# Performance work log

Hardware: AMD Instinct MI355X
Metric: run time of the kernel (lower is better)

Reference implementation:

```python
import jax, jax.numpy as jnp
import numpy as np

EMBED_DIM = 1024
NUM_HEADS = 16
HEAD_DIM = EMBED_DIM // NUM_HEADS
BITS = 8


def quantize_bits(x, bits):
    # Faithful min-max fake quantization from the original module.
    qmax = 2 ** bits - 1
    x_min = x.min()
    x_max = x.max()
    scale = (x_max - x_min) / (qmax + 1e-08)
    x_q = jnp.round(jnp.clip((x - x_min) / (scale + 1e-08), 0, qmax))
    return x_q * scale + x_min


def rope_sin_cos(seq_len, dim):
    # inv_freq over half the head dim, matching RotaryEmbedding's freqs table.
    inv_freq = 1.0 / 10000 ** (jnp.arange(0, dim, 2, dtype=jnp.float32) / dim)
    t = jnp.arange(seq_len, dtype=jnp.float32)
    freqs = t[:, None] * inv_freq[None, :]  # (S, D/2)
    return jnp.sin(freqs), jnp.cos(freqs)


def apply_rotary(x, sin, cos):
    # x: (B, H, S, D); sin/cos: (1, 1, S, D/2)
    x1, x2 = jnp.split(x, 2, axis=-1)
    return jnp.concatenate([x1 * cos - x2 * sin, x1 * sin + x2 * cos], axis=-1)


def setup_inputs() -> dict:
    key = jax.random.key(0)
    k1, k2, k3 = jax.random.split(key, 3)
    B, S, E = 2, 2048, EMBED_DIM
    x = jax.random.normal(k1, (B, S, E), dtype=jnp.float32)
    # lecun_normal-style init: std = 1/sqrt(fan_in)
    w_qkv = jax.random.normal(k2, (E, 3 * E), dtype=jnp.float32) / np.sqrt(E)
    w_out = jax.random.normal(k3, (E, E), dtype=jnp.float32) / np.sqrt(E)
    return {"x": x, "w_qkv": w_qkv, "w_out": w_out}


def reference(x, w_qkv, w_out):
    B, S, E = x.shape
    H, D = NUM_HEADS, HEAD_DIM
    # Fake-quantized QKV projection
    qkv = x @ quantize_bits(w_qkv, BITS)                    # (B, S, 3E)
    qkv = qkv.reshape(B, S, 3, H, D)
    q = qkv[:, :, 0].transpose(0, 2, 1, 3)                  # (B, H, S, D)
    k = qkv[:, :, 1].transpose(0, 2, 1, 3)
    v = qkv[:, :, 2].transpose(0, 2, 1, 3)
    sin, cos = rope_sin_cos(S, D)
    sin = sin[None, None]
    cos = cos[None, None]
    q = apply_rotary(q, sin, cos)
    k = apply_rotary(k, sin, cos)
    scores = jnp.einsum('bhqd,bhkd->bhqk', q, k) / jnp.sqrt(jnp.float32(D))
    attn = jax.nn.softmax(scores, axis=-1)                  # (B, H, S, S)
    out = jnp.einsum('bhqk,bhkd->bhqd', attn, v)            # (B, H, S, D)
    out = out.transpose(0, 2, 1, 3).reshape(B, S, E)
    return out @ quantize_bits(w_out, BITS)
```

## Files before the change

kernel.cpp:

```cpp
#include <hip/hip_runtime.h>
#include <hip/hip_bf16.h>

typedef __bf16 bf16;
typedef bf16  bf16x8 __attribute__((ext_vector_type(8)));
typedef bf16  bf16x4 __attribute__((ext_vector_type(4)));
typedef bf16  bf16x2 __attribute__((ext_vector_type(2)));
typedef float f32x4  __attribute__((ext_vector_type(4)));
typedef float f32x16 __attribute__((ext_vector_type(16)));
typedef int   i32x4  __attribute__((ext_vector_type(4)));

#define MFMA16(a,b,c) __builtin_amdgcn_mfma_f32_16x16x32_bf16((a),(b),(c),0,0,0)
#define MFMA32(a,b,c) __builtin_amdgcn_mfma_f32_32x32x16_bf16((a),(b),(c),0,0,0)

#define GLDS16(gp, lp) __builtin_amdgcn_global_load_lds( \
    (const __attribute__((address_space(1))) void*)(void*)(gp), \
    (__attribute__((address_space(3))) void*)(lp), 16, 0, 0)

static __device__ __forceinline__ bf16x8 lds_frag(const char* p){
  i32x4 v = *(const i32x4*)p;
  return __builtin_bit_cast(bf16x8, v);
}
static __device__ __forceinline__ bf16x8 g_frag(const bf16* p){
  i32x4 v = *(const i32x4*)p;
  return __builtin_bit_cast(bf16x8, v);
}
static __device__ __forceinline__ unsigned pk_bf16(float a, float b){
  bf16x2 v = { (bf16)a, (bf16)b };
  return __builtin_bit_cast(unsigned, v);
}
static __device__ __forceinline__ void p32swap(unsigned &a, unsigned &b){
  asm("v_permlane32_swap_b32 %0, %1" : "+v"(a), "+v"(b));
}

__device__ __forceinline__ unsigned fmap(float f){
  unsigned u = __float_as_uint(f);
  return (u & 0x80000000u) ? ~u : (u | 0x80000000u);
}
__device__ __forceinline__ float funmap(unsigned m){
  unsigned u = (m & 0x80000000u) ? (m & 0x7FFFFFFFu) : ~m;
  return __uint_as_float(u);
}

__global__ void init_mm(unsigned* mm){
  if (threadIdx.x == 0){
    mm[0] = 0xFFFFFFFFu; mm[1] = 0u;
    mm[2] = 0xFFFFFFFFu; mm[3] = 0u;
  }
}

__global__ void minmax_k(const float* __restrict__ w, int n, unsigned* __restrict__ mm){
  __shared__ unsigned smn[256], smx[256];
  int tid = threadIdx.x;
  unsigned lmn = 0xFFFFFFFFu, lmx = 0u;
  for (int i = blockIdx.x * blockDim.x + tid; i < n; i += gridDim.x * blockDim.x){
    unsigned u = fmap(w[i]);
    lmn = min(lmn, u); lmx = max(lmx, u);
  }
  smn[tid] = lmn; smx[tid] = lmx;
  __syncthreads();
  for (int s = 128; s > 0; s >>= 1){
    if (tid < s){
      smn[tid] = min(smn[tid], smn[tid + s]);
      smx[tid] = max(smx[tid], smx[tid + s]);
    }
    __syncthreads();
  }
  if (tid == 0){ atomicMin(&mm[0], smn[0]); atomicMax(&mm[1], smx[0]); }
}

__global__ void dq_t(const float* __restrict__ w, bf16* __restrict__ wt,
                     int R, int C, const unsigned* __restrict__ mm){
  __shared__ float t[32][33];
  float xmin = funmap(mm[0]);
  float xmax = funmap(mm[1]);
  float scale = (xmax - xmin) / 255.0f;
  float denom = scale + 1e-8f;
  int ct = blockIdx.x * 32, rt = blockIdx.y * 32;
  int tx = threadIdx.x, ty = threadIdx.y;
#pragma unroll
  for (int p = 0; p < 4; ++p){
    int r = rt + p * 8 + ty;
    float x = w[(size_t)r * C + ct + tx];
    float q = rintf(fminf(fmaxf((x - xmin) / denom, 0.0f), 255.0f));
    t[p * 8 + ty][tx] = q * scale + xmin;
  }
  __syncthreads();
#pragma unroll
  for (int p = 0; p < 4; ++p){
    int c = p * 8 + ty;
    wt[(size_t)(ct + c) * R + rt + tx] = (bf16)t[tx][c];
  }
}

__global__ void cast_x(const float* __restrict__ x, bf16* __restrict__ xb, int n4){
  int i = blockIdx.x * 256 + threadIdx.x;
  if (i < n4){
    f32x4 v = *(const f32x4*)(x + (size_t)i * 4);
    bf16x4 o = { (bf16)v.x, (bf16)v.y, (bf16)v.z, (bf16)v.w };
    *(bf16x4*)(xb + (size_t)i * 4) = o;
  }
}

__global__ void sincos_k(float* __restrict__ sintab, float* __restrict__ costab){
  int idx = blockIdx.x * 256 + threadIdx.x;
  int i = idx & 31, s = idx >> 5;
  float invf = powf(10000.0f, -(float)i / 32.0f);
  float fr = (float)s * invf;
  sintab[idx] = sinf(fr);
  costab[idx] = cosf(fr);
}

__global__ void rope_qk(const float* __restrict__ qkv,
                        const float* __restrict__ sintab, const float* __restrict__ costab,
                        bf16* __restrict__ Qr, bf16* __restrict__ Kr){
  int idx = blockIdx.x * 256 + threadIdx.x;
  int i  = idx & 31;
  int s  = (idx >> 5) & 2047;
  int bh = idx >> 16;
  int b = bh >> 4, h = bh & 15;
  const float QS = 0.18033688011f;
  const float* row = qkv + (size_t)(b * 2048 + s) * 3072 + h * 64;
  float q1 = row[i],        q2 = row[32 + i];
  float k1 = row[1024 + i], k2 = row[1024 + 32 + i];
  float sn = sintab[s * 32 + i], cs = costab[s * 32 + i];
  size_t o = ((size_t)bh * 2048 + s) * 64 + i;
  Qr[o]      = (bf16)((q1 * cs - q2 * sn) * QS);
  Qr[o + 32] = (bf16)((q1 * sn + q2 * cs) * QS);
  Kr[o]      = (bf16)(k1 * cs - k2 * sn);
  Kr[o + 32] = (bf16)(k1 * sn + k2 * cs);
}

__global__ void vtrans(const float* __restrict__ qkv, bf16* __restrict__ Vt){
  __shared__ float t[64][65];
  int bh = blockIdx.x >> 5;
  int st = (blockIdx.x & 31) * 64;
  int b = bh >> 4, h = bh & 15;
  int tx = threadIdx.x & 63, ty4 = threadIdx.x >> 6;
#pragma unroll
  for (int p = 0; p < 16; ++p){
    int s = p * 4 + ty4;
    t[s][tx] = qkv[(size_t)(b * 2048 + st + s) * 3072 + 2048 + h * 64 + tx];
  }
  __syncthreads();
#pragma unroll
  for (int p = 0; p < 16; ++p){
    int d = p * 4 + ty4;
    Vt[((size_t)bh * 64 + d) * 2048 + st + tx] = (bf16)t[tx][d];
  }
}

__global__ __launch_bounds__(256, 2) void gemm_bt(
    const bf16* __restrict__ A, const bf16* __restrict__ Bt,
    float* __restrict__ C, int M, int N, int K)
{
  __shared__ __align__(16) char lds[32768];
  int nbx = N >> 7;
  int bid = blockIdx.x;
  int nwg = gridDim.x;
  if ((nwg & 7) == 0){ int q = nwg >> 3; bid = (bid & 7) * q + (bid >> 3); }
  int row0 = (bid / nbx) << 7;
  int col0 = (bid % nbx) << 7;
  int tid = threadIdx.x, lane = tid & 63, wid = tid >> 6;
  int wr = (wid >> 1) * 64, wc = (wid & 1) * 64;
  int lr = lane & 15, g = lane >> 4;

  int aoff[2][4], boff[2][4];
#pragma unroll
  for (int kk = 0; kk < 2; ++kk){
#pragma unroll
    for (int m = 0; m < 4; ++m){
      int ra = wr + m * 16 + lr;
      aoff[kk][m] = ra * 128 + ((((kk * 4 + g) ^ ((ra >> 1) & 7))) << 4);
      int rb = wc + m * 16 + lr;
      boff[kk][m] = 16384 + rb * 128 + ((((kk * 4 + g) ^ ((rb >> 1) & 7))) << 4);
    }
  }

  const bf16* pA[4]; const bf16* pB[4]; int loff[4];
#pragma unroll
  for (int is = 0; is < 4; ++is){
    int f = is * 4096 + wid * 1024 + lane * 16;
    int r = f >> 7, c = (f >> 4) & 7;
    int cg = c ^ ((r >> 1) & 7);
    pA[is] = A  + (size_t)(row0 + r) * K + cg * 8;
    pB[is] = Bt + (size_t)(col0 + r) * K + cg * 8;
    loff[is] = is * 4096 + wid * 1024;
  }

  f32x4 acc[4][4] = {};
  for (int kt = 0; kt < K; kt += 64){
    __syncthreads();
#pragma unroll
    for (int is = 0; is < 4; ++is){
      GLDS16(pA[is] + kt, lds + loff[is]);
      GLDS16(pB[is] + kt, lds + 16384 + loff[is]);
    }
    __syncthreads();
#pragma unroll
    for (int kk = 0; kk < 2; ++kk){
      bf16x8 af[4], bfb[4];
#pragma unroll
      for (int m = 0; m < 4; ++m) af[m] = lds_frag(lds + aoff[kk][m]);
#pragma unroll
      for (int n = 0; n < 4; ++n) bfb[n] = lds_frag(lds + boff[kk][n]);
#pragma unroll
      for (int m = 0; m < 4; ++m)
#pragma unroll
        for (int n = 0; n < 4; ++n)
          acc[m][n] = MFMA16(af[m], bfb[n], acc[m][n]);
    }
  }

#pragma unroll
  for (int m = 0; m < 4; ++m){
    int row = row0 + wr + m * 16 + g * 4;
#pragma unroll
    for (int n = 0; n < 4; ++n){
      int col = col0 + wc + n * 16 + lr;
      float* cp = C + (size_t)row * N + col;
#pragma unroll
      for (int r = 0; r < 4; ++r)
        cp[(size_t)r * N] = acc[m][n][r];
    }
  }
}

__global__ __launch_bounds__(256, 2) void attn_k(
    const bf16* __restrict__ Q, const bf16* __restrict__ K,
    const bf16* __restrict__ Vt, bf16* __restrict__ AO)
{
  __shared__ __align__(16) char kl[8192];
  __shared__ __align__(16) char vl[8192];

  int bid = blockIdx.x;
  bid = (bid & 7) * 64 + (bid >> 3);
  int bh = bid >> 4, qblk = bid & 15;
  int b = bh >> 4, h = bh & 15;
  int tid = threadIdx.x, lane = tid & 63, wid = tid >> 6;
  int l31 = lane & 31, hi = lane >> 5, hi8 = hi * 8;
  int q0 = qblk * 128 + wid * 32;

  const bf16* Qb = Q  + ((size_t)bh * 2048 + q0) * 64;
  const bf16* Kb = K  + (size_t)bh * 2048 * 64;
  const bf16* Vb = Vt + (size_t)bh * 64 * 2048;

  bf16x8 qf[4];
#pragma unroll
  for (int t = 0; t < 4; ++t)
    qf[t] = g_frag(Qb + (size_t)l31 * 64 + t * 16 + hi8);

  const bf16* pKs[2]; const bf16* pVs[2]; int ldo[2];
#pragma unroll
  for (int is = 0; is < 2; ++is){
    int f = wid * 2048 + is * 1024 + lane * 16;
    int r = f >> 7;
    int cg = ((f >> 4) & 7) ^ (r & 7);
    pKs[is] = Kb + (size_t)r * 64 + cg * 8;
    pVs[is] = Vb + (size_t)r * 2048 + cg * 8;
    ldo[is] = wid * 2048 + is * 1024;
  }

  f32x16 o0 = {}, o1 = {};
  float mrun = -1e30f, lrun = 0.0f;

  for (int c = 0; c < 32; ++c){
    int kv0 = c * 64;
    __syncthreads();
#pragma unroll
    for (int is = 0; is < 2; ++is){
      GLDS16(pKs[is] + (size_t)kv0 * 64, kl + ldo[is]);
      GLDS16(pVs[is] + kv0,              vl + ldo[is]);
    }
    __syncthreads();

#pragma unroll
    for (int kk = 0; kk < 2; ++kk){
      int krow = kk * 32 + l31;
      bf16x8 kf[4], vfr[4];
#pragma unroll
      for (int t = 0; t < 4; ++t)
        kf[t] = lds_frag(kl + krow * 128 + ((((2 * t + hi) ^ (krow & 7))) << 4));
#pragma unroll
      for (int u = 0; u < 4; ++u){
        int d = (u & 1) * 32 + l31;
        vfr[u] = lds_frag(vl + d * 128 +
                          ((((kk * 4) + ((u >> 1) * 2) + hi) ^ (d & 7)) << 4));
      }
      f32x16 sc = {};
#pragma unroll
      for (int t = 0; t < 4; ++t) sc = MFMA32(kf[t], qf[t], sc);

      float a0 = fmaxf(sc[0], sc[1]),   a1 = fmaxf(sc[2], sc[3]);
      float a2 = fmaxf(sc[4], sc[5]),   a3 = fmaxf(sc[6], sc[7]);
      float a4 = fmaxf(sc[8], sc[9]),   a5 = fmaxf(sc[10], sc[11]);
      float a6 = fmaxf(sc[12], sc[13]), a7 = fmaxf(sc[14], sc[15]);
      a0 = fmaxf(a0, a1); a2 = fmaxf(a2, a3);
      a4 = fmaxf(a4, a5); a6 = fmaxf(a6, a7);
      float mt = fmaxf(fmaxf(a0, a2), fmaxf(a4, a6));
      if (!__all(mt - mrun <= 8.0f)){
        mt = fmaxf(mt, __shfl_xor(mt, 32));
        float mn = fmaxf(mrun, mt);
        float cr = __builtin_amdgcn_exp2f(mrun - mn);
#pragma unroll
        for (int r = 0; r < 16; ++r){ o0[r] *= cr; o1[r] *= cr; }
        lrun *= cr; mrun = mn;
      }
#pragma unroll
      for (int r = 0; r < 16; ++r) sc[r] = __builtin_amdgcn_exp2f(sc[r] - mrun);
      float s0 = (sc[0] + sc[1]) + (sc[2] + sc[3]);
      float s1 = (sc[4] + sc[5]) + (sc[6] + sc[7]);
      float s2 = (sc[8] + sc[9]) + (sc[10] + sc[11]);
      float s3 = (sc[12] + sc[13]) + (sc[14] + sc[15]);
      lrun += (s0 + s1) + (s2 + s3);

#pragma unroll
      for (int kh = 0; kh < 2; ++kh){
        unsigned pa0 = pk_bf16(sc[kh * 8 + 0], sc[kh * 8 + 1]);
        unsigned pa1 = pk_bf16(sc[kh * 8 + 2], sc[kh * 8 + 3]);
        unsigned pb0 = pk_bf16(sc[kh * 8 + 4], sc[kh * 8 + 5]);
        unsigned pb1 = pk_bf16(sc[kh * 8 + 6], sc[kh * 8 + 7]);
        p32swap(pa0, pb0); p32swap(pa1, pb1);
        i32x4 wv = { (int)pa0, (int)pa1, (int)pb0, (int)pb1 };
        bf16x8 pf = __builtin_bit_cast(bf16x8, wv);
        o0 = MFMA32(vfr[kh * 2 + 0], pf, o0);
        o1 = MFMA32(vfr[kh * 2 + 1], pf, o1);
      }
    }
  }

  float lt = lrun + __shfl_xor(lrun, 32);
  float inv = 1.0f / lt;
  size_t row = (size_t)b * 2048 + q0 + l31;
  bf16* op = AO + row * 1024 + h * 64 + hi * 4;
#pragma unroll
  for (int qd = 0; qd < 4; ++qd){
    bf16x4 w0 = { (bf16)(o0[qd*4+0]*inv), (bf16)(o0[qd*4+1]*inv),
                  (bf16)(o0[qd*4+2]*inv), (bf16)(o0[qd*4+3]*inv) };
    *(bf16x4*)(op + qd * 8) = w0;
    bf16x4 w1 = { (bf16)(o1[qd*4+0]*inv), (bf16)(o1[qd*4+1]*inv),
                  (bf16)(o1[qd*4+2]*inv), (bf16)(o1[qd*4+3]*inv) };
    *(bf16x4*)(op + 32 + qd * 8) = w1;
  }
}

extern "C" void kernel_launch(void* const* d_in, const int* in_sizes, int n_in,
                              void* d_out, int out_size, void* d_ws, size_t ws_size,
                              hipStream_t stream) {
  const float* x     = (const float*)d_in[0];
  const float* w_qkv = (const float*)d_in[1];
  const float* w_out = (const float*)d_in[2];
  float* out = (float*)d_out;

  char* ws = (char*)d_ws;
  const size_t MB = 1u << 20;
  unsigned* mm   = (unsigned*)(ws);
  float* sintab  = (float*)(ws + 256);
  float* costab  = (float*)(ws + 256 + 262144);
  bf16* xb       = (bf16*)(ws + 1 * MB);
  bf16* wqkvT    = (bf16*)(ws + 9 * MB);
  bf16* woutT    = (bf16*)(ws + 15 * MB);
  float* qkvf    = (float*)(ws + 17 * MB);
  bf16* Qr       = (bf16*)(ws + 65 * MB);
  bf16* Kr       = (bf16*)(ws + 73 * MB);
  bf16* Vt       = (bf16*)(ws + 81 * MB);
  bf16* AO       = (bf16*)(ws + 1 * MB);

  init_mm<<<1, 64, 0, stream>>>(mm);
  minmax_k<<<512, 256, 0, stream>>>(w_qkv, 1024 * 3072, mm);
  minmax_k<<<512, 256, 0, stream>>>(w_out, 1024 * 1024, mm + 2);
  sincos_k<<<256, 256, 0, stream>>>(sintab, costab);
  cast_x<<<4096, 256, 0, stream>>>(x, xb, 4194304 / 4);
  dq_t<<<dim3(96, 32), dim3(32, 8), 0, stream>>>(w_qkv, wqkvT, 1024, 3072, mm);
  dq_t<<<dim3(32, 32), dim3(32, 8), 0, stream>>>(w_out, woutT, 1024, 1024, mm + 2);
  gemm_bt<<<768, 256, 0, stream>>>(xb, wqkvT, qkvf, 4096, 3072, 1024);
  rope_qk<<<8192, 256, 0, stream>>>(qkvf, sintab, costab, Qr, Kr);
  vtrans<<<1024, 256, 0, stream>>>(qkvf, Vt);
  attn_k<<<512, 256, 0, stream>>>(Qr, Kr, Vt, AO);
  gemm_bt<<<256, 256, 0, stream>>>(AO, woutT, out, 4096, 1024, 1024);

  (void)in_sizes; (void)n_in; (void)out_size; (void)ws_size;
}
```

Measured before the change: 171.9 us.

## Fuse RoPE into QKV GEMM epilogue and split attention KV across waves

```diff
diff --git a/kernel.cpp b/kernel.cpp
--- a/kernel.cpp
+++ b/kernel.cpp
@@ -101,45 +101,24 @@
   }
 }
 
-__global__ void sincos_k(float* __restrict__ sintab, float* __restrict__ costab){
+__global__ void sincos_k(float2* __restrict__ sctab){
   int idx = blockIdx.x * 256 + threadIdx.x;
   int i = idx & 31, s = idx >> 5;
   float invf = powf(10000.0f, -(float)i / 32.0f);
   float fr = (float)s * invf;
-  sintab[idx] = sinf(fr);
-  costab[idx] = cosf(fr);
-}
-
-__global__ void rope_qk(const float* __restrict__ qkv,
-                        const float* __restrict__ sintab, const float* __restrict__ costab,
-                        bf16* __restrict__ Qr, bf16* __restrict__ Kr){
-  int idx = blockIdx.x * 256 + threadIdx.x;
-  int i  = idx & 31;
-  int s  = (idx >> 5) & 2047;
-  int bh = idx >> 16;
-  int b = bh >> 4, h = bh & 15;
-  const float QS = 0.18033688011f;
-  const float* row = qkv + (size_t)(b * 2048 + s) * 3072 + h * 64;
-  float q1 = row[i],        q2 = row[32 + i];
-  float k1 = row[1024 + i], k2 = row[1024 + 32 + i];
-  float sn = sintab[s * 32 + i], cs = costab[s * 32 + i];
-  size_t o = ((size_t)bh * 2048 + s) * 64 + i;
-  Qr[o]      = (bf16)((q1 * cs - q2 * sn) * QS);
-  Qr[o + 32] = (bf16)((q1 * sn + q2 * cs) * QS);
-  Kr[o]      = (bf16)(k1 * cs - k2 * sn);
-  Kr[o + 32] = (bf16)(k1 * sn + k2 * cs);
-}
-
-__global__ void vtrans(const float* __restrict__ qkv, bf16* __restrict__ Vt){
+  float2 cs; cs.x = cosf(fr); cs.y = sinf(fr);
+  sctab[idx] = cs;
+}
+
+__global__ void vtrans_b(const bf16* __restrict__ Vraw, bf16* __restrict__ Vt){
   __shared__ float t[64][65];
   int bh = blockIdx.x >> 5;
   int st = (blockIdx.x & 31) * 64;
-  int b = bh >> 4, h = bh & 15;
   int tx = threadIdx.x & 63, ty4 = threadIdx.x >> 6;
 #pragma unroll
   for (int p = 0; p < 16; ++p){
     int s = p * 4 + ty4;
-    t[s][tx] = qkv[(size_t)(b * 2048 + st + s) * 3072 + 2048 + h * 64 + tx];
+    t[s][tx] = (float)Vraw[((size_t)bh * 2048 + st + s) * 64 + tx];
   }
   __syncthreads();
 #pragma unroll
@@ -225,51 +204,161 @@
   }
 }
 
-__global__ __launch_bounds__(256, 2) void attn_k(
+__global__ __launch_bounds__(256, 2) void gemm_qkv(
+    const bf16* __restrict__ A, const bf16* __restrict__ Bt,
+    const float2* __restrict__ sctab,
+    bf16* __restrict__ Qr, bf16* __restrict__ Kr, bf16* __restrict__ Vraw,
+    int M, int N, int K)
+{
+  __shared__ __align__(16) char lds[32768];
+  int nbx = N >> 7;
+  int bid = blockIdx.x;
+  int nwg = gridDim.x;
+  if ((nwg & 7) == 0){ int q = nwg >> 3; bid = (bid & 7) * q + (bid >> 3); }
+  int row0 = (bid / nbx) << 7;
+  int col0 = (bid % nbx) << 7;
+  int tid = threadIdx.x, lane = tid & 63, wid = tid >> 6;
+  int wr = (wid >> 1) * 64, wc = (wid & 1) * 64;
+  int lr = lane & 15, g = lane >> 4;
+
+  int aoff[2][4], boff[2][4];
+#pragma unroll
+  for (int kk = 0; kk < 2; ++kk){
+#pragma unroll
+    for (int m = 0; m < 4; ++m){
+      int ra = wr + m * 16 + lr;
+      aoff[kk][m] = ra * 128 + ((((kk * 4 + g) ^ ((ra >> 1) & 7))) << 4);
+      int rb = wc + m * 16 + lr;
+      boff[kk][m] = 16384 + rb * 128 + ((((kk * 4 + g) ^ ((rb >> 1) & 7))) << 4);
+    }
+  }
+
+  const bf16* pA[4]; const bf16* pB[4]; int loff[4];
+#pragma unroll
+  for (int is = 0; is < 4; ++is){
+    int f = is * 4096 + wid * 1024 + lane * 16;
+    int r = f >> 7, c = (f >> 4) & 7;
+    int cg = c ^ ((r >> 1) & 7);
+    pA[is] = A  + (size_t)(row0 + r) * K + cg * 8;
+    pB[is] = Bt + (size_t)(col0 + r) * K + cg * 8;
+    loff[is] = is * 4096 + wid * 1024;
+  }
+
+  f32x4 acc[4][4] = {};
+  for (int kt = 0; kt < K; kt += 64){
+    __syncthreads();
+#pragma unroll
+    for (int is = 0; is < 4; ++is){
+      GLDS16(pA[is] + kt, lds + loff[is]);
+      GLDS16(pB[is] + kt, lds + 16384 + loff[is]);
+    }
+    __syncthreads();
+#pragma unroll
+    for (int kk = 0; kk < 2; ++kk){
+      bf16x8 af[4], bfb[4];
+#pragma unroll
+      for (int m = 0; m < 4; ++m) af[m] = lds_frag(lds + aoff[kk][m]);
+#pragma unroll
+      for (int n = 0; n < 4; ++n) bfb[n] = lds_frag(lds + boff[kk][n]);
+#pragma unroll
+      for (int m = 0; m < 4; ++m)
+#pragma unroll
+        for (int n = 0; n < 4; ++n)
+          acc[m][n] = MFMA16(af[m], bfb[n], acc[m][n]);
+    }
+  }
+
+  int head = (col0 + wc) >> 6;
+  int sect = head >> 4;
+  int h = head & 15;
+  const float QS = 0.18033688011f;
+
+  if (sect == 2){
+#pragma unroll
+    for (int m = 0; m < 4; ++m){
+#pragma unroll
+      for (int r = 0; r < 4; ++r){
+        int s = row0 + wr + m * 16 + g * 4 + r;
+        int b = s >> 11, s2 = s & 2047;
+        bf16* vp = Vraw + (((size_t)(b * 16 + h)) * 2048 + s2) * 64;
+#pragma unroll
+        for (int n = 0; n < 4; ++n)
+          vp[n * 16 + lr] = (bf16)acc[m][n][r];
+      }
+    }
+  } else {
+    bf16* dst = sect ? Kr : Qr;
+    float scl = sect ? 1.0f : QS;
+#pragma unroll
+    for (int m = 0; m < 4; ++m){
+#pragma unroll
+      for (int r = 0; r < 4; ++r){
+        int s = row0 + wr + m * 16 + g * 4 + r;
+        int b = s >> 11, s2 = s & 2047;
+        bf16* qp = dst + (((size_t)(b * 16 + h)) * 2048 + s2) * 64;
+#pragma unroll
+        for (int n = 0; n < 2; ++n){
+          float x1 = acc[m][n][r], x2 = acc[m][n + 2][r];
+          float2 cs = sctab[s2 * 32 + n * 16 + lr];
+          qp[n * 16 + lr]      = (bf16)((x1 * cs.x - x2 * cs.y) * scl);
+          qp[n * 16 + lr + 32] = (bf16)((x1 * cs.y + x2 * cs.x) * scl);
+        }
+      }
+    }
+  }
+}
+
+__global__ __launch_bounds__(256, 4) void attn_k(
     const bf16* __restrict__ Q, const bf16* __restrict__ K,
     const bf16* __restrict__ Vt, bf16* __restrict__ AO)
 {
-  __shared__ __align__(16) char kl[8192];
-  __shared__ __align__(16) char vl[8192];
+  __shared__ __align__(16) char SB[32768];
+  __shared__ float mlds[4][2][32];
+  __shared__ float invL[2][32];
 
   int bid = blockIdx.x;
-  bid = (bid & 7) * 64 + (bid >> 3);
-  int bh = bid >> 4, qblk = bid & 15;
+  bid = (bid & 7) * 128 + (bid >> 3);
+  int bh = bid >> 5, qb = bid & 31;
   int b = bh >> 4, h = bh & 15;
   int tid = threadIdx.x, lane = tid & 63, wid = tid >> 6;
   int l31 = lane & 31, hi = lane >> 5, hi8 = hi * 8;
-  int q0 = qblk * 128 + wid * 32;
+  int qt = wid >> 1, half = wid & 1;
+  int q0 = qb * 64 + qt * 32;
 
   const bf16* Qb = Q  + ((size_t)bh * 2048 + q0) * 64;
   const bf16* Kb = K  + (size_t)bh * 2048 * 64;
   const bf16* Vb = Vt + (size_t)bh * 64 * 2048;
+  const bf16* Kh = Kb + (size_t)half * 1024 * 64;
+  int vcol0 = half * 1024;
 
   bf16x8 qf[4];
 #pragma unroll
   for (int t = 0; t < 4; ++t)
     qf[t] = g_frag(Qb + (size_t)l31 * 64 + t * 16 + hi8);
 
-  const bf16* pKs[2]; const bf16* pVs[2]; int ldo[2];
-#pragma unroll
-  for (int is = 0; is < 2; ++is){
-    int f = wid * 2048 + is * 1024 + lane * 16;
+  const bf16* pKs[4]; const bf16* pVs[4]; int ldo[4];
+#pragma unroll
+  for (int is = 0; is < 4; ++is){
+    int f = qt * 4096 + is * 1024 + lane * 16;
     int r = f >> 7;
     int cg = ((f >> 4) & 7) ^ (r & 7);
-    pKs[is] = Kb + (size_t)r * 64 + cg * 8;
-    pVs[is] = Vb + (size_t)r * 2048 + cg * 8;
-    ldo[is] = wid * 2048 + is * 1024;
-  }
+    pKs[is] = Kh + (size_t)r * 64 + cg * 8;
+    pVs[is] = Vb + (size_t)r * 2048 + vcol0 + cg * 8;
+    ldo[is] = qt * 4096 + is * 1024;
+  }
+  char* klh = SB + half * 8192;
+  char* vlh = SB + 16384 + half * 8192;
 
   f32x16 o0 = {}, o1 = {};
   float mrun = -1e30f, lrun = 0.0f;
 
-  for (int c = 0; c < 32; ++c){
+  for (int c = 0; c < 16; ++c){
     int kv0 = c * 64;
     __syncthreads();
 #pragma unroll
-    for (int is = 0; is < 2; ++is){
-      GLDS16(pKs[is] + (size_t)kv0 * 64, kl + ldo[is]);
-      GLDS16(pVs[is] + kv0,              vl + ldo[is]);
+    for (int is = 0; is < 4; ++is){
+      GLDS16(pKs[is] + (size_t)kv0 * 64, klh + ldo[is]);
+      GLDS16(pVs[is] + kv0,              vlh + ldo[is]);
     }
     __syncthreads();
 
@@ -279,11 +368,11 @@
       bf16x8 kf[4], vfr[4];
 #pragma unroll
       for (int t = 0; t < 4; ++t)
-        kf[t] = lds_frag(kl + krow * 128 + ((((2 * t + hi) ^ (krow & 7))) << 4));
+        kf[t] = lds_frag(klh + krow * 128 + ((((2 * t + hi) ^ (krow & 7))) << 4));
 #pragma unroll
       for (int u = 0; u < 4; ++u){
         int d = (u & 1) * 32 + l31;
-        vfr[u] = lds_frag(vl + d * 128 +
+        vfr[u] = lds_frag(vlh + d * 128 +
                           ((((kk * 4) + ((u >> 1) * 2) + hi) ^ (d & 7)) << 4));
       }
       f32x16 sc = {};
@@ -328,19 +417,45 @@
     }
   }
 
-  float lt = lrun + __shfl_xor(lrun, 32);
-  float inv = 1.0f / lt;
-  size_t row = (size_t)b * 2048 + q0 + l31;
-  bf16* op = AO + row * 1024 + h * 64 + hi * 4;
-#pragma unroll
-  for (int qd = 0; qd < 4; ++qd){
-    bf16x4 w0 = { (bf16)(o0[qd*4+0]*inv), (bf16)(o0[qd*4+1]*inv),
-                  (bf16)(o0[qd*4+2]*inv), (bf16)(o0[qd*4+3]*inv) };
-    *(bf16x4*)(op + qd * 8) = w0;
-    bf16x4 w1 = { (bf16)(o1[qd*4+0]*inv), (bf16)(o1[qd*4+1]*inv),
-                  (bf16)(o1[qd*4+2]*inv), (bf16)(o1[qd*4+3]*inv) };
-    *(bf16x4*)(op + 32 + qd * 8) = w1;
-  }
+  lrun += __shfl_xor(lrun, 32);
+
+  __syncthreads();
+  if (lane < 32){ mlds[wid][0][l31] = mrun; mlds[wid][1][l31] = lrun; }
+  __syncthreads();
+  float mp = mlds[wid ^ 1][0][l31];
+  float M = fmaxf(mrun, mp);
+  float ew = __builtin_amdgcn_exp2f(mrun - M);
+  if (half == 0 && lane < 32){
+    float lp = mlds[wid ^ 1][1][l31];
+    invL[qt][l31] = 1.0f / (lrun * ew + lp * __builtin_amdgcn_exp2f(mp - M));
+  }
+  float* Ow = (float*)SB + wid * 2048;
+#pragma unroll
+  for (int r = 0; r < 16; ++r){
+    int d = 8 * (r >> 2) + 4 * hi + (r & 3);
+    Ow[d * 32 + l31]        = o0[r] * ew;
+    Ow[(d + 32) * 32 + l31] = o1[r] * ew;
+  }
+  __syncthreads();
+  int qt2 = tid >> 7, qf31 = tid & 31, dseg = (tid >> 5) & 3;
+  const float* Oa = (float*)SB + (2 * qt2) * 2048;
+  const float* Ob = (float*)SB + (2 * qt2 + 1) * 2048;
+  float iL = invL[qt2][qf31];
+  bf16* outp = AO + ((size_t)(b * 2048 + qb * 64 + qt2 * 32 + qf31)) * 1024
+                  + h * 64 + dseg * 16;
+  bf16x8 w0, w1;
+#pragma unroll
+  for (int j = 0; j < 8; ++j){
+    int d = dseg * 16 + j;
+    w0[j] = (bf16)((Oa[d * 32 + qf31] + Ob[d * 32 + qf31]) * iL);
+  }
+#pragma unroll
+  for (int j = 0; j < 8; ++j){
+    int d = dseg * 16 + 8 + j;
+    w1[j] = (bf16)((Oa[d * 32 + qf31] + Ob[d * 32 + qf31]) * iL);
+  }
+  *(bf16x8*)outp = w0;
+  *(bf16x8*)(outp + 8) = w1;
 }
 
 extern "C" void kernel_launch(void* const* d_in, const int* in_sizes, int n_in,
@@ -354,12 +469,11 @@
   char* ws = (char*)d_ws;
   const size_t MB = 1u << 20;
   unsigned* mm   = (unsigned*)(ws);
-  float* sintab  = (float*)(ws + 256);
-  float* costab  = (float*)(ws + 256 + 262144);
+  float2* sctab  = (float2*)(ws + 256);
   bf16* xb       = (bf16*)(ws + 1 * MB);
   bf16* wqkvT    = (bf16*)(ws + 9 * MB);
   bf16* woutT    = (bf16*)(ws + 15 * MB);
-  float* qkvf    = (float*)(ws + 17 * MB);
+  bf16* Vraw     = (bf16*)(ws + 17 * MB);
   bf16* Qr       = (bf16*)(ws + 65 * MB);
   bf16* Kr       = (bf16*)(ws + 73 * MB);
   bf16* Vt       = (bf16*)(ws + 81 * MB);
@@ -368,14 +482,13 @@
   init_mm<<<1, 64, 0, stream>>>(mm);
   minmax_k<<<512, 256, 0, stream>>>(w_qkv, 1024 * 3072, mm);
   minmax_k<<<512, 256, 0, stream>>>(w_out, 1024 * 1024, mm + 2);
-  sincos_k<<<256, 256, 0, stream>>>(sintab, costab);
+  sincos_k<<<256, 256, 0, stream>>>(sctab);
   cast_x<<<4096, 256, 0, stream>>>(x, xb, 4194304 / 4);
   dq_t<<<dim3(96, 32), dim3(32, 8), 0, stream>>>(w_qkv, wqkvT, 1024, 3072, mm);
   dq_t<<<dim3(32, 32), dim3(32, 8), 0, stream>>>(w_out, woutT, 1024, 1024, mm + 2);
-  gemm_bt<<<768, 256, 0, stream>>>(xb, wqkvT, qkvf, 4096, 3072, 1024);
-  rope_qk<<<8192, 256, 0, stream>>>(qkvf, sintab, costab, Qr, Kr);
-  vtrans<<<1024, 256, 0, stream>>>(qkvf, Vt);
-  attn_k<<<512, 256, 0, stream>>>(Qr, Kr, Vt, AO);
+  gemm_qkv<<<768, 256, 0, stream>>>(xb, wqkvT, sctab, Qr, Kr, Vraw, 4096, 3072, 1024);
+  vtrans_b<<<1024, 256, 0, stream>>>(Vraw, Vt);
+  attn_k<<<1024, 256, 0, stream>>>(Qr, Kr, Vt, AO);
   gemm_bt<<<256, 256, 0, stream>>>(AO, woutT, out, 4096, 1024, 1024);
 
   (void)in_sizes; (void)n_in; (void)out_size; (void)ws_size;
```

New measurement: 163.0 us. 5.2% less time.
